# Kernel optimization log

Measured on AMD Instinct MI355X. Metric: run time of the kernel, lower is better.

Reference implementation:

```python
import jax, jax.numpy as jnp
import numpy as np


def _sample_plane(plane, gx, gy):
    """Bilinear sample plane (C,H,W) at normalized coords gx,gy in [-1,1],
    align_corners=True (matches F.grid_sample). gx indexes W, gy indexes H.
    gx, gy: (M,). Returns (C, M)."""
    C, H, W = plane.shape
    ix = (gx + 1.0) * 0.5 * (W - 1)
    iy = (gy + 1.0) * 0.5 * (H - 1)
    ix0f = jnp.floor(ix)
    iy0f = jnp.floor(iy)
    wx1 = ix - ix0f
    wy1 = iy - iy0f
    wx0 = 1.0 - wx1
    wy0 = 1.0 - wy1
    x0 = jnp.clip(ix0f.astype(jnp.int32), 0, W - 1)
    x1 = jnp.clip(ix0f.astype(jnp.int32) + 1, 0, W - 1)
    y0 = jnp.clip(iy0f.astype(jnp.int32), 0, H - 1)
    y1 = jnp.clip(iy0f.astype(jnp.int32) + 1, 0, H - 1)
    flat = plane.reshape(C, H * W)  # (C, H*W)
    v00 = jnp.take(flat, y0 * W + x0, axis=1)
    v01 = jnp.take(flat, y0 * W + x1, axis=1)
    v10 = jnp.take(flat, y1 * W + x0, axis=1)
    v11 = jnp.take(flat, y1 * W + x1, axis=1)
    return v00 * (wy0 * wx0) + v01 * (wy0 * wx1) + v10 * (wy1 * wx0) + v11 * (wy1 * wx1)


def setup_inputs() -> dict:
    key = jax.random.key(0)
    ks = jax.random.split(key, 10)
    B, N = 1, 524288
    C3, RES = 144, 512  # triplane_c*3, plane resolution
    HID = 256
    sw = lambda fan: 1.0 / np.sqrt(fan)
    return {
        "points": jax.random.uniform(ks[0], (B, N, 3), dtype=jnp.float32),  # grid coords in [0,1]
        "triplanes": jax.random.normal(ks[1], (C3, RES, RES), dtype=jnp.float32),
        "w0": jax.random.normal(ks[2], (HID, C3), dtype=jnp.float32) * sw(C3),
        "b0": jax.random.normal(ks[3], (HID,), dtype=jnp.float32) * 0.01,
        "w1": jax.random.normal(ks[4], (HID, HID), dtype=jnp.float32) * sw(HID),
        "b1": jax.random.normal(ks[5], (HID,), dtype=jnp.float32) * 0.01,
        "w2": jax.random.normal(ks[6], (HID, HID), dtype=jnp.float32) * sw(HID),
        "b2": jax.random.normal(ks[7], (HID,), dtype=jnp.float32) * 0.01,
        "wa": jax.random.normal(ks[8], (1, HID), dtype=jnp.float32) * sw(HID),
        "ba": jax.random.normal(ks[9], (1,), dtype=jnp.float32) * 0.01,
    }


def reference(points, triplanes, w0, b0, w1, b1, w2, b2, wa, ba):
    B, N, _ = points.shape
    # bilinear_sample_triplanes: map [0,1] -> [-1,1] (the points*2-1 inside the method)
    g = points.reshape(B * N, 3) * 2.0 - 1.0
    x, y, z = g[:, 0], g[:, 1], g[:, 2]
    plane_xy, plane_yz, plane_xz = jnp.split(triplanes, 3, axis=0)  # each (48, H, W)
    # grid_sample grid is (x_width, y_height): grid xy=[x,y], xz=[x,z], yz=[y,z]
    xy_f = _sample_plane(plane_xy, x, y)  # (48, B*N)
    xz_f = _sample_plane(plane_xz, x, z)
    yz_f = _sample_plane(plane_yz, y, z)
    feats = jnp.concatenate([xy_f, yz_f, xz_f], axis=0)  # (144, B*N), torch cat order
    # 1x1 Conv1d chain with ReLU (actvn)
    net = jax.nn.relu(jnp.einsum('oc,cn->on', w0, feats) + b0[:, None])
    net = jax.nn.relu(jnp.einsum('oc,cn->on', w1, net) + b1[:, None])
    net = jax.nn.relu(jnp.einsum('oc,cn->on', w2, net) + b2[:, None])
    alpha = jnp.einsum('oc,cn->on', wa, net) + ba[:, None]  # (1, B*N)
    # alpha_fc output (B,1,N) -> transpose(1,2) -> (B,N,1)
    return alpha.reshape(B, 1, N).transpose(0, 2, 1)
```

## Files before the change

### kernel.cpp

```cpp
#include <hip/hip_runtime.h>
#include <hip/hip_bf16.h>
#include <stdint.h>

typedef __bf16 bf16x8 __attribute__((ext_vector_type(8)));
typedef float f32x4 __attribute__((ext_vector_type(4)));
typedef unsigned short u16;
typedef u16 u16x8 __attribute__((ext_vector_type(8)));
typedef uint32_t u32x4 __attribute__((ext_vector_type(4)));

#define RES 512
#define C3 144
#define CPP 48
#define HID 256
#define TPB 128
#define K0 160
#define BK_PAD 264
#define PLANE_ELEMS ((size_t)RES * RES * CPP)
#define NPTS 524288
#define NBLK (NPTS / TPB)
#define L0_U16 (HID * K0)
#define L12_U16 (HID * HID)
#define L1_IMG L0_U16
#define L2_IMG (L0_U16 + L12_U16)
#define WIMG_U16 (L0_U16 + 2 * L12_U16)

static __device__ __forceinline__ float bf2f(u16 u) {
    uint32_t x = ((uint32_t)u) << 16;
    union { uint32_t i; float f; } c; c.i = x; return c.f;
}
static __device__ __forceinline__ u16 f2bf(float f) {
    __bf16 h = (__bf16)f;
    return __builtin_bit_cast(u16, h);
}

__global__ __launch_bounds__(256) void k_transpose(const float* __restrict__ tri,
                                                   u16* __restrict__ planes) {
    int id = blockIdx.x * 256 + threadIdx.x;
    int p = id >> 18;
    int rem = id & ((1 << 18) - 1);
    int y = rem >> 9, x = rem & (RES - 1);
    const float* src = tri + ((size_t)p * CPP) * (RES * RES) + (size_t)y * RES + x;
    u16 outv[CPP] __attribute__((aligned(16)));
    #pragma unroll
    for (int c = 0; c < CPP; ++c)
        outv[c] = f2bf(src[(size_t)c * (RES * RES)]);
    u16* dst = planes + (size_t)id * CPP;
    #pragma unroll
    for (int j = 0; j < 6; ++j)
        ((u32x4*)dst)[j] = ((const u32x4*)outv)[j];
}

__global__ __launch_bounds__(256) void k_prep_w(const float* __restrict__ w0,
                                                const float* __restrict__ w1,
                                                const float* __restrict__ w2,
                                                u16* __restrict__ wimg) {
    int id = blockIdx.x * 256 + threadIdx.x;
    if (id < L0_U16) {
        int j = id & 7;
        int f = id >> 3;
        int lane = f & 63;
        int g2 = f >> 6;
        int mf = g2 & 1;
        int t2 = g2 >> 1;
        int kb = t2 % 5;
        int w  = t2 / 5;
        int m = w * 32 + mf * 16 + (lane & 15);
        int k = kb * 32 + (lane >> 4) * 8 + j;
        wimg[id] = f2bf(k < C3 ? w0[m * C3 + k] : 0.f);
    }
    {
        int j = id & 7;
        int f = id >> 3;
        int lane = f & 63;
        int g2 = f >> 6;
        int mf = g2 & 1;
        int t2 = g2 >> 1;
        int kb = t2 & 7;
        int w  = t2 >> 3;
        int m = w * 32 + mf * 16 + (lane & 15);
        int k = kb * 32 + (lane >> 4) * 8 + j;
        wimg[L1_IMG + id] = f2bf(w1[m * HID + k]);
        wimg[L2_IMG + id] = f2bf(w2[m * HID + k]);
    }
}

template<int NKB>
static __device__ __forceinline__ void do_kbloop(
    const u16* __restrict__ wl, const u16* buf, f32x4 (&acc)[2][8],
    int wave, int lane)
{
    const int r = lane & 15;
    const int g = lane >> 4;
    #pragma unroll
    for (int kb = 0; kb < NKB; ++kb) {
        bf16x8 a[2];
        #pragma unroll
        for (int mf = 0; mf < 2; ++mf)
            a[mf] = *(const bf16x8*)(wl + ((size_t)((wave * NKB + kb) * 2 + mf)) * 512 + lane * 8);
        #pragma unroll
        for (int h = 0; h < 2; ++h) {
            bf16x8 b[4];
            #pragma unroll
            for (int nf = 0; nf < 4; ++nf)
                b[nf] = *(const bf16x8*)(buf + ((h * 4 + nf) * 16 + r) * BK_PAD + kb * 32 + g * 8);
            #pragma unroll
            for (int mf = 0; mf < 2; ++mf)
                #pragma unroll
                for (int nf = 0; nf < 4; ++nf)
                    acc[mf][h * 4 + nf] = __builtin_amdgcn_mfma_f32_16x16x32_bf16(
                        a[mf], b[nf], acc[mf][h * 4 + nf], 0, 0, 0);
        }
    }
}

static __device__ __forceinline__ void epilogue(
    f32x4 (&acc)[2][8], const float* __restrict__ bias,
    u16* buf, int wave, int lane)
{
    const int r = lane & 15;
    const int g = lane >> 4;
    #pragma unroll
    for (int mf = 0; mf < 2; ++mf) {
        int mb = wave * 32 + mf * 16 + g * 4;
        f32x4 bb = *(const f32x4*)(bias + mb);
        #pragma unroll
        for (int nf = 0; nf < 8; ++nf) {
            int n = nf * 16 + r;
            union { u16 u[4]; unsigned long long v; } pk;
            #pragma unroll
            for (int q = 0; q < 4; ++q) {
                float v = acc[mf][nf][q] + bb[q];
                pk.u[q] = f2bf(v > 0.0f ? v : 0.0f);
            }
            *(unsigned long long*)(buf + n * BK_PAD + mb) = pk.v;
        }
    }
}

__global__ __launch_bounds__(512)
__attribute__((amdgpu_waves_per_eu(4, 4)))
void k_fused(
    const float* __restrict__ points,
    const u16* __restrict__ planes,
    const u16* __restrict__ wimg,
    const float* __restrict__ b0, const float* __restrict__ b1,
    const float* __restrict__ b2,
    const float* __restrict__ wa, const float* __restrict__ ba,
    float* __restrict__ outp)
{
    __shared__ u16 buf[TPB * BK_PAD];
    __shared__ uint32_t soffs[3][4][TPB];
    __shared__ float    swts[3][4][TPB];
    const int t = threadIdx.x;
    const int lane = t & 63;
    const int wave = t >> 6;
    const int r = lane & 15;
    const int g = lane >> 4;
    const int p0 = blockIdx.x * TPB;

    if (t < TPB) {
        u32x4 z = {0, 0, 0, 0};
        *(u32x4*)&buf[t * BK_PAD + 144] = z;
        *(u32x4*)&buf[t * BK_PAD + 152] = z;
    }

    if (t < 3 * TPB) {
        const int pln = t >> 7;
        const int pt  = t & (TPB - 1);
        const float* pp = points + (size_t)(p0 + pt) * 3;
        float px = pp[0] * 2.f - 1.f;
        float py = pp[1] * 2.f - 1.f;
        float pz = pp[2] * 2.f - 1.f;
        float gx, gy;
        if (pln == 0)      { gx = px; gy = py; }
        else if (pln == 1) { gx = py; gy = pz; }
        else               { gx = px; gy = pz; }
        float ix = (gx + 1.f) * 0.5f * (float)(RES - 1);
        float iy = (gy + 1.f) * 0.5f * (float)(RES - 1);
        float fx = floorf(ix), fy = floorf(iy);
        float wx1 = ix - fx, wy1 = iy - fy;
        int x0 = ::min(::max((int)fx, 0), RES - 1);
        int x1 = ::min(::max((int)fx + 1, 0), RES - 1);
        int y0 = ::min(::max((int)fy, 0), RES - 1);
        int y1 = ::min(::max((int)fy + 1, 0), RES - 1);
        soffs[pln][0][pt] = (uint32_t)(y0 * RES + x0) * (CPP * 2);
        soffs[pln][1][pt] = (uint32_t)(y0 * RES + x1) * (CPP * 2);
        soffs[pln][2][pt] = (uint32_t)(y1 * RES + x0) * (CPP * 2);
        soffs[pln][3][pt] = (uint32_t)(y1 * RES + x1) * (CPP * 2);
        swts[pln][0][pt] = (1.f - wy1) * (1.f - wx1);
        swts[pln][1][pt] = (1.f - wy1) * wx1;
        swts[pln][2][pt] = wy1 * (1.f - wx1);
        swts[pln][3][pt] = wy1 * wx1;
    }
    __syncthreads();

    #pragma unroll
    for (int rr = 0; rr < 5; ++rr) {
        int task = rr * 512 + t;
        if (task < TPB * 18) {
            int pt = task / 18;
            int rem = task - pt * 18;
            int pi = rem / 6;
            int ch = rem - pi * 6;
            const char* pl = (const char*)planes + (size_t)pi * (PLANE_ELEMS * 2);
            uint32_t co = (uint32_t)ch * 16;
            u16x8 v0 = *(const u16x8*)(pl + soffs[pi][0][pt] + co);
            u16x8 v1 = *(const u16x8*)(pl + soffs[pi][1][pt] + co);
            u16x8 v2 = *(const u16x8*)(pl + soffs[pi][2][pt] + co);
            u16x8 v3 = *(const u16x8*)(pl + soffs[pi][3][pt] + co);
            float W0 = swts[pi][0][pt];
            float W1 = swts[pi][1][pt];
            float W2 = swts[pi][2][pt];
            float W3 = swts[pi][3][pt];
            u16x8 res;
            #pragma unroll
            for (int j = 0; j < 8; ++j) {
                float v = W0 * bf2f(v0[j]) + W1 * bf2f(v1[j])
                        + W2 * bf2f(v2[j]) + W3 * bf2f(v3[j]);
                res[j] = f2bf(v);
            }
            *(u16x8*)&buf[pt * BK_PAD + pi * CPP + ch * 8] = res;
        }
    }
    __syncthreads();

    {
        f32x4 acc[2][8] = {{}};
        do_kbloop<5>(wimg, buf, acc, wave, lane);
        __syncthreads();
        epilogue(acc, b0, buf, wave, lane);
        __syncthreads();
    }
    {
        f32x4 acc[2][8] = {{}};
        do_kbloop<8>(wimg + L1_IMG, buf, acc, wave, lane);
        __syncthreads();
        epilogue(acc, b1, buf, wave, lane);
        __syncthreads();
    }

    {
        f32x4 acc[2][8] = {{}};
        do_kbloop<8>(wimg + L2_IMG, buf, acc, wave, lane);
        float pa[8];
        #pragma unroll
        for (int nf = 0; nf < 8; ++nf) pa[nf] = 0.f;
        #pragma unroll
        for (int mf = 0; mf < 2; ++mf) {
            int mb = wave * 32 + mf * 16 + g * 4;
            f32x4 bb = *(const f32x4*)(b2 + mb);
            f32x4 wv = *(const f32x4*)(wa + mb);
            #pragma unroll
            for (int nf = 0; nf < 8; ++nf) {
                #pragma unroll
                for (int q = 0; q < 4; ++q) {
                    float v = acc[mf][nf][q] + bb[q];
                    pa[nf] += wv[q] * (v > 0.f ? v : 0.f);
                }
            }
        }
        #pragma unroll
        for (int nf = 0; nf < 8; ++nf) {
            pa[nf] += __shfl_xor(pa[nf], 16, 64);
            pa[nf] += __shfl_xor(pa[nf], 32, 64);
        }
        float* part = &swts[0][0][0];
        if (g == 0) {
            #pragma unroll
            for (int nf = 0; nf < 8; ++nf)
                part[wave * TPB + nf * 16 + r] = pa[nf];
        }
        __syncthreads();
        if (t < TPB) {
            float s = ba[0];
            #pragma unroll
            for (int w = 0; w < 8; ++w) s += part[w * TPB + t];
            outp[p0 + t] = s;
        }
    }
}

extern "C" void kernel_launch(void* const* d_in, const int* in_sizes, int n_in,
                              void* d_out, int out_size, void* d_ws, size_t ws_size,
                              hipStream_t stream) {
    const float* points = (const float*)d_in[0];
    const float* tri    = (const float*)d_in[1];
    const float* w0 = (const float*)d_in[2];
    const float* b0 = (const float*)d_in[3];
    const float* w1 = (const float*)d_in[4];
    const float* b1 = (const float*)d_in[5];
    const float* w2 = (const float*)d_in[6];
    const float* b2 = (const float*)d_in[7];
    const float* wa = (const float*)d_in[8];
    const float* ba = (const float*)d_in[9];
    float* outp = (float*)d_out;

    char* wsb = (char*)d_ws;
    u16* planes = (u16*)wsb;
    size_t off = 3 * PLANE_ELEMS * 2;
    u16* wimg = (u16*)(wsb + off);

    k_transpose<<<(3 * RES * RES) / 256, 256, 0, stream>>>(tri, planes);
    k_prep_w<<<256, 256, 0, stream>>>(w0, w1, w2, wimg);
    k_fused<<<NBLK, 512, 0, stream>>>(points, planes, wimg,
                                      b0, b1, b2, wa, ba, outp);
}
```

Before: 256.4 us.

## Retile MLP MFMA waves into 4x2 grid of 64x64 output tiles

Changes the per-wave output tile of the MLP GEMMs from 32 rows by all 128 points to 64 rows by 64 points, arranged as a 4x2 wave grid. Each wave now loads 4 B fragments from LDS per k-step instead of 8, and 4 A fragments from global instead of 2. This halves shared-memory reads of activations and raises global weight-fragment reads. The final alpha reduction is adjusted to sum 4 partials instead of 8.

```diff
diff --git a/kernel.cpp b/kernel.cpp
--- a/kernel.cpp
+++ b/kernel.cpp
@@ -86,46 +86,47 @@
 
 template<int NKB>
 static __device__ __forceinline__ void do_kbloop(
-    const u16* __restrict__ wl, const u16* buf, f32x4 (&acc)[2][8],
-    int wave, int lane)
+    const u16* __restrict__ wl, const u16* buf, f32x4 (&acc)[4][4],
+    int mw, int nw, int lane)
 {
     const int r = lane & 15;
     const int g = lane >> 4;
     #pragma unroll
     for (int kb = 0; kb < NKB; ++kb) {
-        bf16x8 a[2];
-        #pragma unroll
-        for (int mf = 0; mf < 2; ++mf)
-            a[mf] = *(const bf16x8*)(wl + ((size_t)((wave * NKB + kb) * 2 + mf)) * 512 + lane * 8);
+        bf16x8 b[4];
+        #pragma unroll
+        for (int nf = 0; nf < 4; ++nf)
+            b[nf] = *(const bf16x8*)(buf + (nw * 64 + nf * 16 + r) * BK_PAD + kb * 32 + g * 8);
         #pragma unroll
         for (int h = 0; h < 2; ++h) {
-            bf16x8 b[4];
-            #pragma unroll
-            for (int nf = 0; nf < 4; ++nf)
-                b[nf] = *(const bf16x8*)(buf + ((h * 4 + nf) * 16 + r) * BK_PAD + kb * 32 + g * 8);
-            #pragma unroll
-            for (int mf = 0; mf < 2; ++mf)
+            bf16x8 a[2];
+            #pragma unroll
+            for (int m2 = 0; m2 < 2; ++m2)
+                a[m2] = *(const bf16x8*)(wl +
+                    ((size_t)(((mw * 2 + h) * NKB + kb) * 2 + m2)) * 512 + lane * 8);
+            #pragma unroll
+            for (int m2 = 0; m2 < 2; ++m2)
                 #pragma unroll
                 for (int nf = 0; nf < 4; ++nf)
-                    acc[mf][h * 4 + nf] = __builtin_amdgcn_mfma_f32_16x16x32_bf16(
-                        a[mf], b[nf], acc[mf][h * 4 + nf], 0, 0, 0);
+                    acc[h * 2 + m2][nf] = __builtin_amdgcn_mfma_f32_16x16x32_bf16(
+                        a[m2], b[nf], acc[h * 2 + m2][nf], 0, 0, 0);
         }
     }
 }
 
 static __device__ __forceinline__ void epilogue(
-    f32x4 (&acc)[2][8], const float* __restrict__ bias,
-    u16* buf, int wave, int lane)
+    f32x4 (&acc)[4][4], const float* __restrict__ bias,
+    u16* buf, int mw, int nw, int lane)
 {
     const int r = lane & 15;
     const int g = lane >> 4;
     #pragma unroll
-    for (int mf = 0; mf < 2; ++mf) {
-        int mb = wave * 32 + mf * 16 + g * 4;
+    for (int mf = 0; mf < 4; ++mf) {
+        int mb = mw * 64 + mf * 16 + g * 4;
         f32x4 bb = *(const f32x4*)(bias + mb);
         #pragma unroll
-        for (int nf = 0; nf < 8; ++nf) {
-            int n = nf * 16 + r;
+        for (int nf = 0; nf < 4; ++nf) {
+            int n = nw * 64 + nf * 16 + r;
             union { u16 u[4]; unsigned long long v; } pk;
             #pragma unroll
             for (int q = 0; q < 4; ++q) {
@@ -154,6 +155,8 @@
     const int t = threadIdx.x;
     const int lane = t & 63;
     const int wave = t >> 6;
+    const int mw = wave >> 1;
+    const int nw = wave & 1;
     const int r = lane & 15;
     const int g = lane >> 4;
     const int p0 = blockIdx.x * TPB;
@@ -225,33 +228,33 @@
     __syncthreads();
 
     {
-        f32x4 acc[2][8] = {{}};
-        do_kbloop<5>(wimg, buf, acc, wave, lane);
-        __syncthreads();
-        epilogue(acc, b0, buf, wave, lane);
+        f32x4 acc[4][4] = {{}};
+        do_kbloop<5>(wimg, buf, acc, mw, nw, lane);
+        __syncthreads();
+        epilogue(acc, b0, buf, mw, nw, lane);
         __syncthreads();
     }
     {
-        f32x4 acc[2][8] = {{}};
-        do_kbloop<8>(wimg + L1_IMG, buf, acc, wave, lane);
-        __syncthreads();
-        epilogue(acc, b1, buf, wave, lane);
+        f32x4 acc[4][4] = {{}};
+        do_kbloop<8>(wimg + L1_IMG, buf, acc, mw, nw, lane);
+        __syncthreads();
+        epilogue(acc, b1, buf, mw, nw, lane);
         __syncthreads();
     }
 
     {
-        f32x4 acc[2][8] = {{}};
-        do_kbloop<8>(wimg + L2_IMG, buf, acc, wave, lane);
-        float pa[8];
-        #pragma unroll
-        for (int nf = 0; nf < 8; ++nf) pa[nf] = 0.f;
-        #pragma unroll
-        for (int mf = 0; mf < 2; ++mf) {
-            int mb = wave * 32 + mf * 16 + g * 4;
+        f32x4 acc[4][4] = {{}};
+        do_kbloop<8>(wimg + L2_IMG, buf, acc, mw, nw, lane);
+        float pa[4];
+        #pragma unroll
+        for (int nf = 0; nf < 4; ++nf) pa[nf] = 0.f;
+        #pragma unroll
+        for (int mf = 0; mf < 4; ++mf) {
+            int mb = mw * 64 + mf * 16 + g * 4;
             f32x4 bb = *(const f32x4*)(b2 + mb);
             f32x4 wv = *(const f32x4*)(wa + mb);
             #pragma unroll
-            for (int nf = 0; nf < 8; ++nf) {
+            for (int nf = 0; nf < 4; ++nf) {
                 #pragma unroll
                 for (int q = 0; q < 4; ++q) {
                     float v = acc[mf][nf][q] + bb[q];
@@ -260,21 +263,21 @@
             }
         }
         #pragma unroll
-        for (int nf = 0; nf < 8; ++nf) {
+        for (int nf = 0; nf < 4; ++nf) {
             pa[nf] += __shfl_xor(pa[nf], 16, 64);
             pa[nf] += __shfl_xor(pa[nf], 32, 64);
         }
         float* part = &swts[0][0][0];
         if (g == 0) {
             #pragma unroll
-            for (int nf = 0; nf < 8; ++nf)
-                part[wave * TPB + nf * 16 + r] = pa[nf];
+            for (int nf = 0; nf < 4; ++nf)
+                part[mw * TPB + nw * 64 + nf * 16 + r] = pa[nf];
         }
         __syncthreads();
         if (t < TPB) {
             float s = ba[0];
             #pragma unroll
-            for (int w = 0; w < 8; ++w) s += part[w * TPB + t];
+            for (int w = 0; w < 4; ++w) s += part[w * TPB + t];
             outp[p0 + t] = s;
         }
     }
```

New measurement: 353.4 us. +37.8%, slower.

## Make fused kernel persistent over tiles and prefetch next tile's gather during MLP

Applied to the files above, without the earlier changes.

Each block now processes 16 point tiles in a loop with double-buffered LDS. The next tile's bilinear gather loads are issued into registers before the current tile's MLP runs, then resolved into the other buffer after layer 0. This aims to hide the gather memory latency behind the MFMA work. In exchange, register pressure rises, occupancy drops to 2 waves per EU, LDS doubles and the grid shrinks to 256 blocks, which may hurt latency hiding and load balance.

```diff
diff --git a/kernel.cpp b/kernel.cpp
--- a/kernel.cpp
+++ b/kernel.cpp
@@ -17,7 +17,9 @@
 #define BK_PAD 264
 #define PLANE_ELEMS ((size_t)RES * RES * CPP)
 #define NPTS 524288
-#define NBLK (NPTS / TPB)
+#define TILES 16
+#define GRID (NPTS / (TPB * TILES))
+#define GTASKS (TPB * 18)
 #define L0_U16 (HID * K0)
 #define L12_U16 (HID * HID)
 #define L1_IMG L0_U16
@@ -137,8 +139,84 @@
     }
 }
 
+static __device__ __forceinline__ void gather_issue(
+    const float* __restrict__ points, const u16* __restrict__ planes,
+    int p0n, int t,
+    float (&hix)[5], float (&hiy)[5],
+    u16x8 (&hc0)[5], u16x8 (&hc1)[5], u16x8 (&hc2)[5], u16x8 (&hc3)[5])
+{
+    #pragma unroll
+    for (int rr = 0; rr < 5; ++rr) {
+        int task = rr * 512 + t;
+        if (task < GTASKS) {
+            int pt = task / 18;
+            int rem = task - pt * 18;
+            int pi = rem / 6;
+            int ch = rem - pi * 6;
+            const float* pp = points + (size_t)(p0n + pt) * 3;
+            float px = pp[0] * 2.f - 1.f;
+            float py = pp[1] * 2.f - 1.f;
+            float pz = pp[2] * 2.f - 1.f;
+            float gx = (pi == 1) ? py : px;
+            float gy = (pi == 0) ? py : pz;
+            float ix = (gx + 1.f) * 0.5f * (float)(RES - 1);
+            float iy = (gy + 1.f) * 0.5f * (float)(RES - 1);
+            hix[rr] = ix; hiy[rr] = iy;
+            float fx = floorf(ix), fy = floorf(iy);
+            int x0 = ::min(::max((int)fx, 0), RES - 1);
+            int x1 = ::min(::max((int)fx + 1, 0), RES - 1);
+            int y0 = ::min(::max((int)fy, 0), RES - 1);
+            int y1 = ::min(::max((int)fy + 1, 0), RES - 1);
+            const u16* pl = planes + (size_t)pi * PLANE_ELEMS + ch * 8;
+            hc0[rr] = *(const u16x8*)(pl + (uint32_t)(y0 * RES + x0) * CPP);
+            hc1[rr] = *(const u16x8*)(pl + (uint32_t)(y0 * RES + x1) * CPP);
+            hc2[rr] = *(const u16x8*)(pl + (uint32_t)(y1 * RES + x0) * CPP);
+            hc3[rr] = *(const u16x8*)(pl + (uint32_t)(y1 * RES + x1) * CPP);
+        }
+    }
+}
+
+static __device__ __forceinline__ void gather_resolve(
+    u16* __restrict__ bn, int t,
+    const float (&hix)[5], const float (&hiy)[5],
+    const u16x8 (&hc0)[5], const u16x8 (&hc1)[5],
+    const u16x8 (&hc2)[5], const u16x8 (&hc3)[5])
+{
+    if (t < TPB) {
+        u32x4 z = {0, 0, 0, 0};
+        *(u32x4*)&bn[t * BK_PAD + 144] = z;
+        *(u32x4*)&bn[t * BK_PAD + 152] = z;
+    }
+    #pragma unroll
+    for (int rr = 0; rr < 5; ++rr) {
+        int task = rr * 512 + t;
+        if (task < GTASKS) {
+            int pt = task / 18;
+            int rem = task - pt * 18;
+            int pi = rem / 6;
+            int ch = rem - pi * 6;
+            float ix = hix[rr], iy = hiy[rr];
+            float wx1 = ix - floorf(ix);
+            float wy1 = iy - floorf(iy);
+            float W0 = (1.f - wy1) * (1.f - wx1);
+            float W1 = (1.f - wy1) * wx1;
+            float W2 = wy1 * (1.f - wx1);
+            float W3 = wy1 * wx1;
+            u16x8 v0 = hc0[rr], v1 = hc1[rr], v2 = hc2[rr], v3 = hc3[rr];
+            u16x8 res;
+            #pragma unroll
+            for (int j = 0; j < 8; ++j) {
+                float v = W0 * bf2f(v0[j]) + W1 * bf2f(v1[j])
+                        + W2 * bf2f(v2[j]) + W3 * bf2f(v3[j]);
+                res[j] = f2bf(v);
+            }
+            *(u16x8*)&bn[pt * BK_PAD + pi * CPP + ch * 8] = res;
+        }
+    }
+}
+
 __global__ __launch_bounds__(512)
-__attribute__((amdgpu_waves_per_eu(4, 4)))
+__attribute__((amdgpu_waves_per_eu(2, 2)))
 void k_fused(
     const float* __restrict__ points,
     const u16* __restrict__ planes,
@@ -148,135 +226,88 @@
     const float* __restrict__ wa, const float* __restrict__ ba,
     float* __restrict__ outp)
 {
-    __shared__ u16 buf[TPB * BK_PAD];
-    __shared__ uint32_t soffs[3][4][TPB];
-    __shared__ float    swts[3][4][TPB];
+    __shared__ u16 buf[2][TPB * BK_PAD];
+    __shared__ float part[8 * TPB];
     const int t = threadIdx.x;
     const int lane = t & 63;
     const int wave = t >> 6;
     const int r = lane & 15;
     const int g = lane >> 4;
-    const int p0 = blockIdx.x * TPB;
-
-    if (t < TPB) {
-        u32x4 z = {0, 0, 0, 0};
-        *(u32x4*)&buf[t * BK_PAD + 144] = z;
-        *(u32x4*)&buf[t * BK_PAD + 152] = z;
-    }
-
-    if (t < 3 * TPB) {
-        const int pln = t >> 7;
-        const int pt  = t & (TPB - 1);
-        const float* pp = points + (size_t)(p0 + pt) * 3;
-        float px = pp[0] * 2.f - 1.f;
-        float py = pp[1] * 2.f - 1.f;
-        float pz = pp[2] * 2.f - 1.f;
-        float gx, gy;
-        if (pln == 0)      { gx = px; gy = py; }
-        else if (pln == 1) { gx = py; gy = pz; }
-        else               { gx = px; gy = pz; }
-        float ix = (gx + 1.f) * 0.5f * (float)(RES - 1);
-        float iy = (gy + 1.f) * 0.5f * (float)(RES - 1);
-        float fx = floorf(ix), fy = floorf(iy);
-        float wx1 = ix - fx, wy1 = iy - fy;
-        int x0 = ::min(::max((int)fx, 0), RES - 1);
-        int x1 = ::min(::max((int)fx + 1, 0), RES - 1);
-        int y0 = ::min(::max((int)fy, 0), RES - 1);
-        int y1 = ::min(::max((int)fy + 1, 0), RES - 1);
-        soffs[pln][0][pt] = (uint32_t)(y0 * RES + x0) * (CPP * 2);
-        soffs[pln][1][pt] = (uint32_t)(y0 * RES + x1) * (CPP * 2);
-        soffs[pln][2][pt] = (uint32_t)(y1 * RES + x0) * (CPP * 2);
-        soffs[pln][3][pt] = (uint32_t)(y1 * RES + x1) * (CPP * 2);
-        swts[pln][0][pt] = (1.f - wy1) * (1.f - wx1);
-        swts[pln][1][pt] = (1.f - wy1) * wx1;
-        swts[pln][2][pt] = wy1 * (1.f - wx1);
-        swts[pln][3][pt] = wy1 * wx1;
-    }
+    const int tile0 = blockIdx.x * TILES;
+
+    float hix[5], hiy[5];
+    u16x8 hc0[5], hc1[5], hc2[5], hc3[5];
+
+    gather_issue(points, planes, tile0 * TPB, t, hix, hiy, hc0, hc1, hc2, hc3);
+    gather_resolve(&buf[0][0], t, hix, hiy, hc0, hc1, hc2, hc3);
     __syncthreads();
 
-    #pragma unroll
-    for (int rr = 0; rr < 5; ++rr) {
-        int task = rr * 512 + t;
-        if (task < TPB * 18) {
-            int pt = task / 18;
-            int rem = task - pt * 18;
-            int pi = rem / 6;
-            int ch = rem - pi * 6;
-            const char* pl = (const char*)planes + (size_t)pi * (PLANE_ELEMS * 2);
-            uint32_t co = (uint32_t)ch * 16;
-            u16x8 v0 = *(const u16x8*)(pl + soffs[pi][0][pt] + co);
-            u16x8 v1 = *(const u16x8*)(pl + soffs[pi][1][pt] + co);
-            u16x8 v2 = *(const u16x8*)(pl + soffs[pi][2][pt] + co);
-            u16x8 v3 = *(const u16x8*)(pl + soffs[pi][3][pt] + co);
-            float W0 = swts[pi][0][pt];
-            float W1 = swts[pi][1][pt];
-            float W2 = swts[pi][2][pt];
-            float W3 = swts[pi][3][pt];
-            u16x8 res;
-            #pragma unroll
-            for (int j = 0; j < 8; ++j) {
-                float v = W0 * bf2f(v0[j]) + W1 * bf2f(v1[j])
-                        + W2 * bf2f(v2[j]) + W3 * bf2f(v3[j]);
-                res[j] = f2bf(v);
-            }
-            *(u16x8*)&buf[pt * BK_PAD + pi * CPP + ch * 8] = res;
-        }
-    }
-    __syncthreads();
-
-    {
-        f32x4 acc[2][8] = {{}};
-        do_kbloop<5>(wimg, buf, acc, wave, lane);
-        __syncthreads();
-        epilogue(acc, b0, buf, wave, lane);
-        __syncthreads();
-    }
-    {
-        f32x4 acc[2][8] = {{}};
-        do_kbloop<8>(wimg + L1_IMG, buf, acc, wave, lane);
-        __syncthreads();
-        epilogue(acc, b1, buf, wave, lane);
-        __syncthreads();
-    }
-
-    {
-        f32x4 acc[2][8] = {{}};
-        do_kbloop<8>(wimg + L2_IMG, buf, acc, wave, lane);
-        float pa[8];
-        #pragma unroll
-        for (int nf = 0; nf < 8; ++nf) pa[nf] = 0.f;
-        #pragma unroll
-        for (int mf = 0; mf < 2; ++mf) {
-            int mb = wave * 32 + mf * 16 + g * 4;
-            f32x4 bb = *(const f32x4*)(b2 + mb);
-            f32x4 wv = *(const f32x4*)(wa + mb);
+    int cur = 0;
+    for (int it = 0; it < TILES; ++it) {
+        const u16* bc = &buf[cur][0];
+        u16* bn = &buf[cur ^ 1][0];
+        const int p0 = (tile0 + it) * TPB;
+        const bool pref = (it + 1 < TILES);
+
+        if (pref)
+            gather_issue(points, planes, p0 + TPB, t, hix, hiy, hc0, hc1, hc2, hc3);
+
+        {
+            f32x4 acc[2][8] = {{}};
+            do_kbloop<5>(wimg, bc, acc, wave, lane);
+            __syncthreads();
+            epilogue(acc, b0, (u16*)bc, wave, lane);
+            if (pref)
+                gather_resolve(bn, t, hix, hiy, hc0, hc1, hc2, hc3);
+            __syncthreads();
+        }
+        {
+            f32x4 acc[2][8] = {{}};
+            do_kbloop<8>(wimg + L1_IMG, bc, acc, wave, lane);
+            __syncthreads();
+            epilogue(acc, b1, (u16*)bc, wave, lane);
+            __syncthreads();
+        }
+        {
+            f32x4 acc[2][8] = {{}};
+            do_kbloop<8>(wimg + L2_IMG, bc, acc, wave, lane);
+            float pa[8];
+            #pragma unroll
+            for (int nf = 0; nf < 8; ++nf) pa[nf] = 0.f;
+            #pragma unroll
+            for (int mf = 0; mf < 2; ++mf) {
+                int mb = wave * 32 + mf * 16 + g * 4;
+                f32x4 bb = *(const f32x4*)(b2 + mb);
+                f32x4 wv = *(const f32x4*)(wa + mb);
+                #pragma unroll
+                for (int nf = 0; nf < 8; ++nf) {
+                    #pragma unroll
+                    for (int q = 0; q < 4; ++q) {
+                        float v = acc[mf][nf][q] + bb[q];
+                        pa[nf] += wv[q] * (v > 0.f ? v : 0.f);
+                    }
+                }
+            }
             #pragma unroll
             for (int nf = 0; nf < 8; ++nf) {
+                pa[nf] += __shfl_xor(pa[nf], 16, 64);
+                pa[nf] += __shfl_xor(pa[nf], 32, 64);
+            }
+            if (g == 0) {
                 #pragma unroll
-                for (int q = 0; q < 4; ++q) {
-                    float v = acc[mf][nf][q] + bb[q];
-                    pa[nf] += wv[q] * (v > 0.f ? v : 0.f);
-                }
-            }
-        }
-        #pragma unroll
-        for (int nf = 0; nf < 8; ++nf) {
-            pa[nf] += __shfl_xor(pa[nf], 16, 64);
-            pa[nf] += __shfl_xor(pa[nf], 32, 64);
-        }
-        float* part = &swts[0][0][0];
-        if (g == 0) {
-            #pragma unroll
-            for (int nf = 0; nf < 8; ++nf)
-                part[wave * TPB + nf * 16 + r] = pa[nf];
-        }
-        __syncthreads();
-        if (t < TPB) {
-            float s = ba[0];
-            #pragma unroll
-            for (int w = 0; w < 8; ++w) s += part[w * TPB + t];
-            outp[p0 + t] = s;
-        }
+                for (int nf = 0; nf < 8; ++nf)
+                    part[wave * TPB + nf * 16 + r] = pa[nf];
+            }
+            __syncthreads();
+            if (t < TPB) {
+                float s = ba[0];
+                #pragma unroll
+                for (int w = 0; w < 8; ++w) s += part[w * TPB + t];
+                outp[p0 + t] = s;
+            }
+            __syncthreads();
+        }
+        cur ^= 1;
     }
 }
 
@@ -302,6 +333,6 @@
 
     k_transpose<<<(3 * RES * RES) / 256, 256, 0, stream>>>(tri, planes);
     k_prep_w<<<256, 256, 0, stream>>>(w0, w1, w2, wimg);
-    k_fused<<<NBLK, 512, 0, stream>>>(points, planes, wimg,
+    k_fused<<<GRID, 512, 0, stream>>>(points, planes, wimg,
                                       b0, b1, b2, wa, ba, outp);
 }
```

Result: slower. 688.4 us (+168.5%).
